# Kernel optimization log

Measured on AMD Instinct MI355X. Metric: run time of the kernel, lower is better.

Reference implementation:

```python
import jax, jax.numpy as jnp
import numpy as np

EPS = 1e-7


def setup_inputs() -> dict:
    key = jax.random.key(0)
    k1, k2, k3, k4 = jax.random.split(key, 4)
    N, M = 8192, 8192
    inputs = jax.random.normal(k1, (N, 2), dtype=jnp.float32)
    outputs = jax.random.normal(k2, (N,), dtype=jnp.float32)
    x = jax.random.normal(k3, (M, 2), dtype=jnp.float32)
    # positive per-query bandwidths in [0.5, 1.5)
    bandwidth = 0.5 + jax.random.uniform(k4, (M,), dtype=jnp.float32)
    return {"x": x, "inputs": inputs, "outputs": outputs, "bandwidth": bandwidth}


def reference(x, inputs, outputs, bandwidth):
    # Squared pairwise distances (cdist followed by .pow(2) in the original):
    # d2[n, m] = ||inputs[n] - x[m]||^2, computed via the expansion to avoid
    # materializing an (N, M, 2) intermediate.
    a2 = jnp.sum(inputs * inputs, axis=1)  # (N,)
    b2 = jnp.sum(x * x, axis=1)            # (M,)
    d2 = a2[:, None] + b2[None, :] - 2.0 * (inputs @ x.T)  # (N, M)
    d2 = jnp.maximum(d2, 0.0)

    bw = bandwidth[None, :]  # (1, M), per-query bandwidth
    weights = jnp.exp(-d2 / (2.0 * bw * bw))  # (N, M)
    # Normalization over dim 0 (over the N reference points)
    weights = weights / (jnp.sum(weights, axis=0, keepdims=True) + EPS)
    # weights.T @ outputs -> (M,), Nadaraya-Watson weighted sum
    weighted = weights.T @ outputs  # (M,)
    return weighted
```

## Files before the change

kernel.cpp:

```cpp
#include <hip/hip_runtime.h>

#define EPS 1e-7f
#define LOG2E 1.44269504088896340736f

constexpr int SEGS  = 32;
constexpr int BLOCK = 256;

__global__ __launch_bounds__(BLOCK) void nw_partial(
    const float2* __restrict__ x,
    const float2* __restrict__ inputs,
    const float*  __restrict__ outputs,
    const float*  __restrict__ bw,
    float2*       __restrict__ partial,
    int N, int M)
{
    const int j   = blockIdx.x * BLOCK + threadIdx.x;
    const int seg = blockIdx.y;
    const int per = (N + SEGS - 1) / SEGS;
    const int i0  = seg * per;
    const int i1  = min(N, i0 + per);

    float x0 = 0.f, x1 = 0.f, k = 0.f;
    if (j < M) {
        float2 xj = x[j];
        x0 = xj.x;
        x1 = xj.y;
        float b = bw[j];
        k = -LOG2E / (2.0f * b * b);
    }

    float num = 0.f, den = 0.f;
    #pragma unroll 8
    for (int i = i0; i < i1; ++i) {
        float2 p  = inputs[i];
        float  oi = outputs[i];
        float dx = p.x - x0;
        float dy = p.y - x1;
        float d2 = fmaf(dx, dx, dy * dy);
        float w  = __builtin_amdgcn_exp2f(d2 * k);
        num = fmaf(w, oi, num);
        den += w;
    }

    if (j < M) partial[seg * M + j] = make_float2(num, den);
}

__global__ __launch_bounds__(BLOCK) void nw_finalize(
    const float2* __restrict__ partial,
    float*        __restrict__ out,
    int M)
{
    const int j = blockIdx.x * BLOCK + threadIdx.x;
    if (j >= M) return;
    float num = 0.f, den = 0.f;
    #pragma unroll
    for (int s = 0; s < SEGS; ++s) {
        float2 p = partial[s * M + j];
        num += p.x;
        den += p.y;
    }
    out[j] = num / (den + EPS);
}

extern "C" void kernel_launch(void* const* d_in, const int* in_sizes, int n_in,
                              void* d_out, int out_size, void* d_ws, size_t ws_size,
                              hipStream_t stream) {
    const float2* x       = (const float2*)d_in[0];
    const float2* inputs  = (const float2*)d_in[1];
    const float*  outputs = (const float*) d_in[2];
    const float*  bwv     = (const float*) d_in[3];
    const int N = in_sizes[2];
    const int M = in_sizes[3];
    float*        out     = (float*)d_out;
    float2*       partial = (float2*)d_ws;

    dim3 grid1((M + BLOCK - 1) / BLOCK, SEGS);
    nw_partial<<<grid1, BLOCK, 0, stream>>>(x, inputs, outputs, bwv, partial, N, M);

    dim3 grid2((M + BLOCK - 1) / BLOCK);
    nw_finalize<<<grid2, BLOCK, 0, stream>>>(partial, out, M);
}
```

Before: 79.85 us.

## Pack reference points and expand exponent into per-query FMA coefficients

A new pre-kernel packs each reference point as float4 (x, y, |p|^2, output), so the main loop does one vector load per point. The per-point exponent is rewritten as a chain of FMAs with query-side coefficients folded in ahead of time. The loop now keeps two independent accumulator pairs, and the segment count doubles to give more blocks. The costs are an extra kernel launch, a larger workspace, and a possible loss of precision from the expanded distance form.

```diff
diff --git a/kernel.cpp b/kernel.cpp
--- a/kernel.cpp
+++ b/kernel.cpp
@@ -3,13 +3,25 @@
 #define EPS 1e-7f
 #define LOG2E 1.44269504088896340736f
 
-constexpr int SEGS  = 32;
+constexpr int SEGS  = 64;
 constexpr int BLOCK = 256;
 
-__global__ __launch_bounds__(BLOCK) void nw_partial(
-    const float2* __restrict__ x,
+__global__ __launch_bounds__(BLOCK) void nw_pack(
     const float2* __restrict__ inputs,
     const float*  __restrict__ outputs,
+    float4*       __restrict__ packed,
+    int N)
+{
+    int i = blockIdx.x * BLOCK + threadIdx.x;
+    if (i < N) {
+        float2 p = inputs[i];
+        packed[i] = make_float4(p.x, p.y, fmaf(p.x, p.x, p.y * p.y), outputs[i]);
+    }
+}
+
+__global__ __launch_bounds__(BLOCK) void nw_partial(
+    const float4* __restrict__ packed,
+    const float2* __restrict__ x,
     const float*  __restrict__ bw,
     float2*       __restrict__ partial,
     int N, int M)
@@ -20,29 +32,41 @@
     const int i0  = seg * per;
     const int i1  = min(N, i0 + per);
 
-    float x0 = 0.f, x1 = 0.f, k = 0.f;
+    float c0 = 0.f, c1 = 0.f, c2 = 0.f, c3 = 0.f;
     if (j < M) {
         float2 xj = x[j];
-        x0 = xj.x;
-        x1 = xj.y;
-        float b = bw[j];
-        k = -LOG2E / (2.0f * b * b);
+        float  b  = bw[j];
+        float  k  = -LOG2E / (2.0f * b * b);
+        c0 = k;
+        c1 = -2.0f * k * xj.x;
+        c2 = -2.0f * k * xj.y;
+        c3 = k * fmaf(xj.x, xj.x, xj.y * xj.y);
     }
 
-    float num = 0.f, den = 0.f;
-    #pragma unroll 8
-    for (int i = i0; i < i1; ++i) {
-        float2 p  = inputs[i];
-        float  oi = outputs[i];
-        float dx = p.x - x0;
-        float dy = p.y - x1;
-        float d2 = fmaf(dx, dx, dy * dy);
-        float w  = __builtin_amdgcn_exp2f(d2 * k);
-        num = fmaf(w, oi, num);
-        den += w;
+    float num0 = 0.f, num1 = 0.f, den0 = 0.f, den1 = 0.f;
+    int i = i0;
+    #pragma unroll 4
+    for (; i + 1 < i1; i += 2) {
+        float4 pa = packed[i];
+        float4 pb = packed[i + 1];
+        float ta = fmaf(c0, pa.z, fmaf(c1, pa.x, fmaf(c2, pa.y, c3)));
+        float tb = fmaf(c0, pb.z, fmaf(c1, pb.x, fmaf(c2, pb.y, c3)));
+        float wa = __builtin_amdgcn_exp2f(ta);
+        float wb = __builtin_amdgcn_exp2f(tb);
+        num0 = fmaf(wa, pa.w, num0);
+        num1 = fmaf(wb, pb.w, num1);
+        den0 += wa;
+        den1 += wb;
+    }
+    if (i < i1) {
+        float4 pa = packed[i];
+        float ta = fmaf(c0, pa.z, fmaf(c1, pa.x, fmaf(c2, pa.y, c3)));
+        float wa = __builtin_amdgcn_exp2f(ta);
+        num0 = fmaf(wa, pa.w, num0);
+        den0 += wa;
     }
 
-    if (j < M) partial[seg * M + j] = make_float2(num, den);
+    if (j < M) partial[seg * M + j] = make_float2(num0 + num1, den0 + den1);
 }
 
 __global__ __launch_bounds__(BLOCK) void nw_finalize(
@@ -72,11 +96,14 @@
     const int N = in_sizes[2];
     const int M = in_sizes[3];
     float*        out     = (float*)d_out;
-    float2*       partial = (float2*)d_ws;
+
+    float2* partial = (float2*)d_ws;
+    float4* packed  = (float4*)((char*)d_ws + (size_t)SEGS * M * sizeof(float2));
+
+    nw_pack<<<dim3((N + BLOCK - 1) / BLOCK), BLOCK, 0, stream>>>(inputs, outputs, packed, N);
 
     dim3 grid1((M + BLOCK - 1) / BLOCK, SEGS);
-    nw_partial<<<grid1, BLOCK, 0, stream>>>(x, inputs, outputs, bwv, partial, N, M);
+    nw_partial<<<grid1, BLOCK, 0, stream>>>(packed, x, bwv, partial, N, M);
 
-    dim3 grid2((M + BLOCK - 1) / BLOCK);
-    nw_finalize<<<grid2, BLOCK, 0, stream>>>(partial, out, M);
+    nw_finalize<<<dim3((M + BLOCK - 1) / BLOCK), BLOCK, 0, stream>>>(partial, out, M);
 }
```

Measured after the change: 79.39 us. Within noise of the previous version (-0.6%).

## Fuse partial and finalize into one cooperative kernel with grid sync

Applied to the files above, without the earlier changes.

Merges the per-segment partial-sum kernel and the finalize kernel into a single cooperative launch that uses a grid-wide sync, removing one kernel launch and its gap. It also pre-scales the coordinates by sqrt of the bandwidth factor so each pair costs fewer operations, and splits the accumulators in two to break the FMA dependency chain. The cooperative launch requires all 1024 blocks to be co-resident (4 per CU on 256 CUs), and the grid.sync itself costs something. The pre-scaling slightly changes rounding.

```diff
diff --git a/kernel.cpp b/kernel.cpp
--- a/kernel.cpp
+++ b/kernel.cpp
@@ -1,4 +1,7 @@
 #include <hip/hip_runtime.h>
+#include <hip/hip_cooperative_groups.h>
+
+namespace cg = cooperative_groups;
 
 #define EPS 1e-7f
 #define LOG2E 1.44269504088896340736f
@@ -6,60 +9,78 @@
 constexpr int SEGS  = 32;
 constexpr int BLOCK = 256;
 
-__global__ __launch_bounds__(BLOCK) void nw_partial(
+__global__ __launch_bounds__(BLOCK, 4) void nw_fused(
     const float2* __restrict__ x,
     const float2* __restrict__ inputs,
     const float*  __restrict__ outputs,
     const float*  __restrict__ bw,
     float2*       __restrict__ partial,
+    float*        __restrict__ out,
     int N, int M)
 {
+    cg::grid_group grid = cg::this_grid();
+
     const int j   = blockIdx.x * BLOCK + threadIdx.x;
     const int seg = blockIdx.y;
     const int per = (N + SEGS - 1) / SEGS;
     const int i0  = seg * per;
     const int i1  = min(N, i0 + per);
 
-    float x0 = 0.f, x1 = 0.f, k = 0.f;
+    float r = 0.f, rx0 = 0.f, ry0 = 0.f;
     if (j < M) {
         float2 xj = x[j];
-        x0 = xj.x;
-        x1 = xj.y;
-        float b = bw[j];
-        k = -LOG2E / (2.0f * b * b);
+        float  b  = bw[j];
+        r   = sqrtf(LOG2E / (2.0f * b * b));
+        rx0 = r * xj.x;
+        ry0 = r * xj.y;
     }
 
-    float num = 0.f, den = 0.f;
-    #pragma unroll 8
-    for (int i = i0; i < i1; ++i) {
-        float2 p  = inputs[i];
-        float  oi = outputs[i];
-        float dx = p.x - x0;
-        float dy = p.y - x1;
-        float d2 = fmaf(dx, dx, dy * dy);
-        float w  = __builtin_amdgcn_exp2f(d2 * k);
-        num = fmaf(w, oi, num);
-        den += w;
+    float num0 = 0.f, num1 = 0.f, den0 = 0.f, den1 = 0.f;
+    int i = i0;
+    #pragma unroll 4
+    for (; i + 1 < i1; i += 2) {
+        float2 pa = inputs[i];
+        float2 pb = inputs[i + 1];
+        float  oa = outputs[i];
+        float  ob = outputs[i + 1];
+        float dxa = fmaf(r, pa.x, -rx0);
+        float dya = fmaf(r, pa.y, -ry0);
+        float dxb = fmaf(r, pb.x, -rx0);
+        float dyb = fmaf(r, pb.y, -ry0);
+        float ta  = fmaf(dxa, dxa, dya * dya);
+        float tb  = fmaf(dxb, dxb, dyb * dyb);
+        float wa  = __builtin_amdgcn_exp2f(-ta);
+        float wb  = __builtin_amdgcn_exp2f(-tb);
+        num0 = fmaf(wa, oa, num0);
+        num1 = fmaf(wb, ob, num1);
+        den0 += wa;
+        den1 += wb;
+    }
+    if (i < i1) {
+        float2 pa = inputs[i];
+        float  oa = outputs[i];
+        float dxa = fmaf(r, pa.x, -rx0);
+        float dya = fmaf(r, pa.y, -ry0);
+        float ta  = fmaf(dxa, dxa, dya * dya);
+        float wa  = __builtin_amdgcn_exp2f(-ta);
+        num0 = fmaf(wa, oa, num0);
+        den0 += wa;
     }
 
-    if (j < M) partial[seg * M + j] = make_float2(num, den);
-}
+    if (j < M) partial[(size_t)seg * M + j] = make_float2(num0 + num1, den0 + den1);
 
-__global__ __launch_bounds__(BLOCK) void nw_finalize(
-    const float2* __restrict__ partial,
-    float*        __restrict__ out,
-    int M)
-{
-    const int j = blockIdx.x * BLOCK + threadIdx.x;
-    if (j >= M) return;
-    float num = 0.f, den = 0.f;
-    #pragma unroll
-    for (int s = 0; s < SEGS; ++s) {
-        float2 p = partial[s * M + j];
-        num += p.x;
-        den += p.y;
+    grid.sync();
+
+    if (seg == 0 && j < M) {
+        float num = 0.f, den = 0.f;
+        #pragma unroll
+        for (int s = 0; s < SEGS; ++s) {
+            float2 p = partial[(size_t)s * M + j];
+            num += p.x;
+            den += p.y;
+        }
+        out[j] = num / (den + EPS);
     }
-    out[j] = num / (den + EPS);
 }
 
 extern "C" void kernel_launch(void* const* d_in, const int* in_sizes, int n_in,
@@ -69,14 +90,14 @@
     const float2* inputs  = (const float2*)d_in[1];
     const float*  outputs = (const float*) d_in[2];
     const float*  bwv     = (const float*) d_in[3];
-    const int N = in_sizes[2];
-    const int M = in_sizes[3];
+    int N = in_sizes[2];
+    int M = in_sizes[3];
     float*        out     = (float*)d_out;
     float2*       partial = (float2*)d_ws;
 
-    dim3 grid1((M + BLOCK - 1) / BLOCK, SEGS);
-    nw_partial<<<grid1, BLOCK, 0, stream>>>(x, inputs, outputs, bwv, partial, N, M);
-
-    dim3 grid2((M + BLOCK - 1) / BLOCK);
-    nw_finalize<<<grid2, BLOCK, 0, stream>>>(partial, out, M);
+    dim3 grid((M + BLOCK - 1) / BLOCK, SEGS);
+    dim3 block(BLOCK);
+    void* args[] = { (void*)&x, (void*)&inputs, (void*)&outputs, (void*)&bwv,
+                     (void*)&partial, (void*)&out, (void*)&N, (void*)&M };
+    hipLaunchCooperativeKernel((const void*)nw_fused, grid, block, args, 0, stream);
 }
```

Result: slower. 176.6 us (+121.2%).

## Assign one wavefront per query with shuffle reduction, fusing finalize

Applied to the files above, without the earlier changes.

Each 64-lane wavefront now owns a single query and strides over all reference points, then reduces num and den with xor shuffles. This removes the second finalize kernel and the partial-sum workspace round trip. The bandwidth scale is folded into the coordinates with a square root, so the exponent argument takes fewer instructions per pair. In exchange every lane loads the reference points itself instead of having them broadcast across a block of queries, which increases load traffic per computed pair. It also adds a shuffle reduction at the end of each wavefront.

```diff
diff --git a/kernel.cpp b/kernel.cpp
--- a/kernel.cpp
+++ b/kernel.cpp
@@ -3,63 +3,48 @@
 #define EPS 1e-7f
 #define LOG2E 1.44269504088896340736f
 
-constexpr int SEGS  = 32;
 constexpr int BLOCK = 256;
 
-__global__ __launch_bounds__(BLOCK) void nw_partial(
+__global__ __launch_bounds__(BLOCK) void nw_wave(
     const float2* __restrict__ x,
     const float2* __restrict__ inputs,
     const float*  __restrict__ outputs,
     const float*  __restrict__ bw,
-    float2*       __restrict__ partial,
+    float*        __restrict__ out,
     int N, int M)
 {
-    const int j   = blockIdx.x * BLOCK + threadIdx.x;
-    const int seg = blockIdx.y;
-    const int per = (N + SEGS - 1) / SEGS;
-    const int i0  = seg * per;
-    const int i1  = min(N, i0 + per);
+    const int lane = threadIdx.x & 63;
+    const int j    = blockIdx.x * (BLOCK / 64) + (threadIdx.x >> 6);
 
-    float x0 = 0.f, x1 = 0.f, k = 0.f;
+    float r = 0.f, rx0 = 0.f, ry0 = 0.f;
     if (j < M) {
         float2 xj = x[j];
-        x0 = xj.x;
-        x1 = xj.y;
-        float b = bw[j];
-        k = -LOG2E / (2.0f * b * b);
+        float  b  = bw[j];
+        r   = sqrtf(LOG2E / (2.0f * b * b));
+        rx0 = r * xj.x;
+        ry0 = r * xj.y;
     }
 
     float num = 0.f, den = 0.f;
     #pragma unroll 8
-    for (int i = i0; i < i1; ++i) {
-        float2 p  = inputs[i];
-        float  oi = outputs[i];
-        float dx = p.x - x0;
-        float dy = p.y - x1;
-        float d2 = fmaf(dx, dx, dy * dy);
-        float w  = __builtin_amdgcn_exp2f(d2 * k);
-        num = fmaf(w, oi, num);
+    for (int i = lane; i < N; i += 64) {
+        float2 p = inputs[i];
+        float  o = outputs[i];
+        float dx = fmaf(r, p.x, -rx0);
+        float dy = fmaf(r, p.y, -ry0);
+        float t  = fmaf(dx, dx, dy * dy);
+        float w  = __builtin_amdgcn_exp2f(-t);
+        num = fmaf(w, o, num);
         den += w;
     }
 
-    if (j < M) partial[seg * M + j] = make_float2(num, den);
-}
+    #pragma unroll
+    for (int off = 32; off > 0; off >>= 1) {
+        num += __shfl_xor(num, off, 64);
+        den += __shfl_xor(den, off, 64);
+    }
 
-__global__ __launch_bounds__(BLOCK) void nw_finalize(
-    const float2* __restrict__ partial,
-    float*        __restrict__ out,
-    int M)
-{
-    const int j = blockIdx.x * BLOCK + threadIdx.x;
-    if (j >= M) return;
-    float num = 0.f, den = 0.f;
-    #pragma unroll
-    for (int s = 0; s < SEGS; ++s) {
-        float2 p = partial[s * M + j];
-        num += p.x;
-        den += p.y;
-    }
-    out[j] = num / (den + EPS);
+    if (lane == 0 && j < M) out[j] = num / (den + EPS);
 }
 
 extern "C" void kernel_launch(void* const* d_in, const int* in_sizes, int n_in,
@@ -72,11 +57,8 @@
     const int N = in_sizes[2];
     const int M = in_sizes[3];
     float*        out     = (float*)d_out;
-    float2*       partial = (float2*)d_ws;
 
-    dim3 grid1((M + BLOCK - 1) / BLOCK, SEGS);
-    nw_partial<<<grid1, BLOCK, 0, stream>>>(x, inputs, outputs, bwv, partial, N, M);
-
-    dim3 grid2((M + BLOCK - 1) / BLOCK);
-    nw_finalize<<<grid2, BLOCK, 0, stream>>>(partial, out, M);
+    const int waves_per_block = BLOCK / 64;
+    dim3 grid((M + waves_per_block - 1) / waves_per_block);
+    nw_wave<<<grid, BLOCK, 0, stream>>>(x, inputs, outputs, bwv, out, N, M);
 }
```

After: 96.78 us. 21.2% more time.
